# Optimization experiments

Measured on AMD Instinct MI355X. Metric: run time of the kernel, lower is better.

Reference implementation:

```python
import jax, jax.numpy as jnp
import numpy as np

H = 2            # attention heads
HID = 128        # hidden_channels
NEG_SLOPE = 0.2  # GATConv leaky_relu slope

N_USER, N_POST, N_ENT = 100000, 50000, 20000
TEXT_D, USER_D, ENT_D = 768, 64, 64
E_PUB, E_REP, E_CON, E_INT, E_FOL = 150000, 300000, 200000, 500000, 500000


def _gat(h_src, h_dst, src, dst, Wsrc, Wdst, asrc, adst, bias):
    """PyG GATConv((-1,-1), C, heads=H, concat=False, add_self_loops=False)."""
    n_dst = h_dst.shape[0]
    C = Wsrc.shape[1] // H
    xs = (h_src @ Wsrc).reshape(-1, H, C)          # [Ns,H,C]
    xd = (h_dst @ Wdst).reshape(-1, H, C)          # [Nd,H,C]
    al_s = jnp.einsum('nhc,hc->nh', xs, asrc)      # [Ns,H]
    al_d = jnp.einsum('nhc,hc->nh', xd, adst)      # [Nd,H]
    e = jax.nn.leaky_relu(al_s[src] + al_d[dst], NEG_SLOPE)   # [E,H]
    m = jax.ops.segment_max(e, dst, num_segments=n_dst)
    m = jnp.where(jnp.isfinite(m), m, 0.0)
    ex = jnp.exp(e - m[dst])
    denom = jax.ops.segment_sum(ex, dst, num_segments=n_dst)
    alpha = ex / (denom[dst] + 1e-16)              # per-dst softmax
    msg = xs[src] * alpha[:, :, None]              # [E,H,C]
    out = jax.ops.segment_sum(msg, dst, num_segments=n_dst)   # [Nd,H,C]
    return out.mean(axis=1) + bias                 # concat=False -> head mean


def setup_inputs() -> dict:
    key = jax.random.key(0)
    ks = jax.random.split(key, 24)
    s = 0.05
    d = {
        'post_cls': jax.random.normal(ks[0], (N_POST, TEXT_D), jnp.float32),
        'user_x': jax.random.normal(ks[1], (N_USER, USER_D), jnp.float32),
        'entity_x': jax.random.normal(ks[2], (N_ENT, ENT_D), jnp.float32),
        'Wpost': jax.random.normal(ks[3], (TEXT_D, HID), jnp.float32) * s,
        'bpost': jnp.zeros((HID,), jnp.float32),
        'Wuser': jax.random.normal(ks[4], (USER_D, HID), jnp.float32) * s,
        'buser': jnp.zeros((HID,), jnp.float32),
        'Went': jax.random.normal(ks[5], (ENT_D, HID), jnp.float32) * s,
        'bent': jnp.zeros((HID,), jnp.float32),
        # 2 layers x 5 relations (publish, repost, contain, interact, follow)
        'gat_Wsrc': jax.random.normal(ks[6], (2, 5, HID, H * HID), jnp.float32) * s,
        'gat_Wdst': jax.random.normal(ks[7], (2, 5, HID, H * HID), jnp.float32) * s,
        'gat_asrc': jax.random.normal(ks[8], (2, 5, H, HID), jnp.float32) * s,
        'gat_adst': jax.random.normal(ks[9], (2, 5, H, HID), jnp.float32) * s,
        'gat_bias': jnp.zeros((2, 5, HID), jnp.float32),
        'Wc1': jax.random.normal(ks[10], (HID, HID // 2), jnp.float32) * s,
        'bc1': jnp.zeros((HID // 2,), jnp.float32),
        'Wc2': jax.random.normal(ks[11], (HID // 2, 1), jnp.float32) * s,
        'bc2': jnp.zeros((1,), jnp.float32),
        'pub_src': jax.random.randint(ks[12], (E_PUB,), 0, N_USER, jnp.int32),
        'pub_dst': jax.random.randint(ks[13], (E_PUB,), 0, N_POST, jnp.int32),
        'rep_src': jax.random.randint(ks[14], (E_REP,), 0, N_USER, jnp.int32),
        'rep_dst': jax.random.randint(ks[15], (E_REP,), 0, N_POST, jnp.int32),
        'con_src': jax.random.randint(ks[16], (E_CON,), 0, N_POST, jnp.int32),
        'con_dst': jax.random.randint(ks[17], (E_CON,), 0, N_ENT, jnp.int32),
        'int_src': jax.random.randint(ks[18], (E_INT,), 0, N_USER, jnp.int32),
        'int_dst': jax.random.randint(ks[19], (E_INT,), 0, N_USER, jnp.int32),
        'fol_src': jax.random.randint(ks[20], (E_FOL,), 0, N_USER, jnp.int32),
        'fol_dst': jax.random.randint(ks[21], (E_FOL,), 0, N_USER, jnp.int32),
    }
    return d


def _forward(post_cls, user_x, entity_x, Wpost, bpost, Wuser, buser, Went, bent,
             gat_Wsrc, gat_Wdst, gat_asrc, gat_adst, gat_bias,
             Wc1, bc1, Wc2, bc2, edges):
    h = {
        'post': post_cls @ Wpost + bpost,
        'user': user_x @ Wuser + buser,
        'entity': entity_x @ Went + bent,
    }
    for l in range(2):
        def g(r, h_src, h_dst, src, dst):
            return _gat(h_src, h_dst, src, dst,
                        gat_Wsrc[l, r], gat_Wdst[l, r],
                        gat_asrc[l, r], gat_adst[l, r], gat_bias[l, r])
        # HeteroConv aggr='sum' over edge types sharing a dst node type
        new_post = (g(0, h['user'], h['post'], edges['pub_src'], edges['pub_dst'])
                    + g(1, h['user'], h['post'], edges['rep_src'], edges['rep_dst']))
        new_ent = g(2, h['post'], h['entity'], edges['con_src'], edges['con_dst'])
        new_user = (g(3, h['user'], h['user'], edges['int_src'], edges['int_dst'])
                    + g(4, h['user'], h['user'], edges['fol_src'], edges['fol_dst']))
        h = {'post': jax.nn.relu(new_post),
             'user': jax.nn.relu(new_user),
             'entity': jax.nn.relu(new_ent)}
    # classifier (dropout inactive at inference)
    z = jax.nn.relu(h['post'] @ Wc1 + bc1)
    out = z @ Wc2 + bc2
    return out.squeeze(-1)   # [n_posts]


def reference(post_cls, user_x, entity_x, Wpost, bpost, Wuser, buser, Went, bent,
              gat_Wsrc, gat_Wdst, gat_asrc, gat_adst, gat_bias,
              Wc1, bc1, Wc2, bc2,
              pub_src, pub_dst, rep_src, rep_dst, con_src, con_dst,
              int_src, int_dst, fol_src, fol_dst):
    edges = dict(pub_src=pub_src, pub_dst=pub_dst, rep_src=rep_src, rep_dst=rep_dst,
                 con_src=con_src, con_dst=con_dst, int_src=int_src, int_dst=int_dst,
                 fol_src=fol_src, fol_dst=fol_dst)
    return _forward(post_cls, user_x, entity_x, Wpost, bpost, Wuser, buser, Went, bent,
                    gat_Wsrc, gat_Wdst, gat_asrc, gat_adst, gat_bias,
                    Wc1, bc1, Wc2, bc2, edges)
```

## Files before the change

kernel.cpp:

```cpp
#include <hip/hip_runtime.h>
#include <cstdint>
#include <cstddef>

#define N_USER 100000
#define N_POST 50000
#define TEXT_D 768
#define USER_D 64
#define E_PUB 150000
#define E_REP 300000
#define E_INT 500000
#define E_FOL 500000
#define E_TOT 1450000
#define N_TOT 300000

typedef unsigned short ushort_t;
typedef float f4v __attribute__((ext_vector_type(4)));
typedef short s8v __attribute__((ext_vector_type(8)));
typedef unsigned short u4v __attribute__((ext_vector_type(4)));

__device__ __forceinline__ float leaky(float v) { return v > 0.f ? v : 0.2f * v; }
__device__ __forceinline__ void split_bf(float x, ushort_t& hi, ushort_t& lo) {
  unsigned u = __float_as_uint(x);
  hi = (ushort_t)(u >> 16);
  float r = x - __uint_as_float(u & 0xFFFF0000u);
  lo = (ushort_t)(__float_as_uint(r) >> 16);
}

struct Ptrs4 { const int* p[4]; };

__global__ void wvec_kernel(const float* __restrict__ W, const float* __restrict__ av,
                            float* __restrict__ wv) {
  int b = blockIdx.x;
  int lr = b / 2, h = b % 2;
  const float* Wp = W + ((size_t)lr * 128 * 256) + (size_t)threadIdx.x * 256 + h * 128;
  const float* ap = av + (size_t)(lr * 2 + h) * 128;
  float acc = 0.f;
  for (int c = 0; c < 128; ++c) acc += Wp[c] * ap[c];
  wv[(size_t)(lr * 2 + h) * 128 + threadIdx.x] = acc;
}

__global__ void wt_prep(const float* __restrict__ W, ushort_t* __restrict__ WTh,
                        ushort_t* __restrict__ WTl, int K, int C) {
  int k = blockIdx.x * 256 + threadIdx.x;
  int c = blockIdx.y;
  if (k >= K) return;
  ushort_t h, l;
  split_bf(W[(size_t)k * C + c], h, l);
  WTh[(size_t)c * K + k] = h;
  WTl[(size_t)c * K + k] = l;
}

__global__ void stk_prep(const float* __restrict__ Wa, const float* __restrict__ Wb,
                         ushort_t* __restrict__ STh, ushort_t* __restrict__ STl) {
  int rel = blockIdx.x;
  int c = blockIdx.y;
  int t = threadIdx.x;
  const float* W = rel ? Wb : Wa;
  float v = W[(size_t)(t & 127) * 256 + (size_t)(t >> 7) * 128 + c];
  ushort_t hh, ll;
  split_bf(v, hh, ll);
  size_t idx = (size_t)c * 512 + (size_t)rel * 256 + t;
  STh[idx] = hh;
  STl[idx] = ll;
}

__global__ void bias_sum(const float* __restrict__ gbias, float* __restrict__ BS) {
  int c = threadIdx.x;
  BS[c]       = gbias[0 * 640 + 0 * 128 + c] + gbias[0 * 640 + 1 * 128 + c];
  BS[128 + c] = gbias[0 * 640 + 3 * 128 + c] + gbias[0 * 640 + 4 * 128 + c];
  BS[256 + c] = gbias[1 * 640 + 0 * 128 + c] + gbias[1 * 640 + 1 * 128 + c];
}

template <int CF, bool BIAS, bool RELU>
__global__ __launch_bounds__(256) void gemm_mfma(const float* __restrict__ X,
                                                 const ushort_t* __restrict__ WTh,
                                                 const ushort_t* __restrict__ WTl,
                                                 const float* __restrict__ bv,
                                                 float* __restrict__ Out,
                                                 int N, int K) {
  __shared__ ushort_t Ah[64][32], Al[64][32];
  __shared__ ushort_t Bh[CF * 16][32], Bl[CF * 16][32];
  int t = threadIdx.x;
  int L = t & 63;
  int wv = t >> 6;
  int m = L & 15, quad = L >> 4;
  int row0 = blockIdx.x * 64;

  f4v acc[CF];
#pragma unroll
  for (int cf = 0; cf < CF; ++cf) acc[cf] = (f4v){0.f, 0.f, 0.f, 0.f};

  int nk = K >> 5;
  for (int kb = 0; kb < nk; ++kb) {
    int k0 = kb * 32;
#pragma unroll
    for (int i = 0; i < 2; ++i) {
      int s = t + 256 * i;
      int r = s >> 3, k4 = s & 7;
      int row = row0 + r;
      float4 v = make_float4(0.f, 0.f, 0.f, 0.f);
      if (row < N) v = *(const float4*)(X + (size_t)row * K + k0 + k4 * 4);
      ushort_t hx, lx, hy, ly, hz, lz, hw, lw;
      split_bf(v.x, hx, lx); split_bf(v.y, hy, ly);
      split_bf(v.z, hz, lz); split_bf(v.w, hw, lw);
      u4v h, l;
      h[0] = hx; h[1] = hy; h[2] = hz; h[3] = hw;
      l[0] = lx; l[1] = ly; l[2] = lz; l[3] = lw;
      *(u4v*)&Ah[r][k4 * 4] = h;
      *(u4v*)&Al[r][k4 * 4] = l;
    }
#pragma unroll
    for (int i = 0; i < CF / 4; ++i) {
      int s = t + 256 * i;
      int c = s >> 2, ch = s & 3;
      *(s8v*)&Bh[c][ch * 8] = *(const s8v*)(WTh + (size_t)c * K + k0 + ch * 8);
      *(s8v*)&Bl[c][ch * 8] = *(const s8v*)(WTl + (size_t)c * K + k0 + ch * 8);
    }
    __syncthreads();
    s8v a_h = *(const s8v*)&Ah[wv * 16 + m][quad * 8];
    s8v a_l = *(const s8v*)&Al[wv * 16 + m][quad * 8];
#pragma unroll
    for (int cf = 0; cf < CF; ++cf) {
      s8v b_h = *(const s8v*)&Bh[cf * 16 + m][quad * 8];
      s8v b_l = *(const s8v*)&Bl[cf * 16 + m][quad * 8];
      acc[cf] = __builtin_amdgcn_mfma_f32_16x16x32_bf16(a_h, b_h, acc[cf], 0, 0, 0);
      acc[cf] = __builtin_amdgcn_mfma_f32_16x16x32_bf16(a_h, b_l, acc[cf], 0, 0, 0);
      acc[cf] = __builtin_amdgcn_mfma_f32_16x16x32_bf16(a_l, b_h, acc[cf], 0, 0, 0);
    }
    __syncthreads();
  }

  float bvs[CF];
#pragma unroll
  for (int cf = 0; cf < CF; ++cf) bvs[cf] = BIAS ? bv[cf * 16 + m] : 0.f;
#pragma unroll
  for (int j = 0; j < 4; ++j) {
    int row = row0 + wv * 16 + quad * 4 + j;
    if (row < N) {
      float* o = Out + (size_t)row * (CF * 16) + m;
#pragma unroll
      for (int cf = 0; cf < CF; ++cf) {
        float vv = acc[cf][j] + bvs[cf];
        if (RELU) vv = fmaxf(vv, 0.f);
        o[cf * 16] = vv;
      }
    }
  }
}

__device__ __forceinline__ void rel_of(int g, int& r, int& loc, int& nb) {
  if (g < 450000) {
    if (g < 150000) { r = 0; loc = g;          nb = 0; }
    else            { r = 1; loc = g - 150000; nb = 50000; }
  } else if (g < 950000)  { r = 2; loc = g - 450000;  nb = 100000; }
  else                    { r = 3; loc = g - 950000;  nb = 200000; }
}
__global__ void histc_kernel(Ptrs4 dsts, int* __restrict__ cnt) {
  int g = blockIdx.x * 256 + threadIdx.x;
  if (g >= E_TOT) return;
  int r, loc, nb;
  rel_of(g, r, loc, nb);
  atomicAdd(&cnt[nb + dsts.p[r][loc]], 1);
}
__global__ __launch_bounds__(256) void scan1_kernel(const int* __restrict__ cnt,
                                                    int* __restrict__ excl,
                                                    int* __restrict__ partials, int Nd) {
  __shared__ int sb[256];
  int t = threadIdx.x;
  int base = blockIdx.x * 1024 + t * 4;
  int v[4];
#pragma unroll
  for (int j = 0; j < 4; ++j) v[j] = (base + j < Nd) ? cnt[base + j] : 0;
  int tot = v[0] + v[1] + v[2] + v[3];
  sb[t] = tot;
  __syncthreads();
  for (int off = 1; off < 256; off <<= 1) {
    int x = 0;
    if (t >= off) x = sb[t - off];
    __syncthreads();
    sb[t] += x;
    __syncthreads();
  }
  int ex = sb[t] - tot;
  if (t == 255) partials[blockIdx.x] = sb[t];
  int run = ex;
#pragma unroll
  for (int j = 0; j < 4; ++j) {
    if (base + j < Nd) excl[base + j] = run;
    run += v[j];
  }
}
__global__ __launch_bounds__(512) void scan2_kernel(int* __restrict__ partials, int B) {
  __shared__ int sb[512];
  int t = threadIdx.x;
  int v = (t < B) ? partials[t] : 0;
  sb[t] = v;
  __syncthreads();
  for (int off = 1; off < 512; off <<= 1) {
    int x = 0;
    if (t >= off) x = sb[t - off];
    __syncthreads();
    sb[t] += x;
    __syncthreads();
  }
  if (t < B) partials[t] = sb[t] - v;
}
__global__ void scan3_kernel(const int* __restrict__ excl, const int* __restrict__ partials,
                             int* __restrict__ rowptr, int* __restrict__ cursor) {
  int i = blockIdx.x * 256 + threadIdx.x;
  if (i < N_TOT) {
    int v = excl[i] + partials[i >> 10];
    rowptr[i] = v;
    cursor[i] = v;
  }
  if (i == 0) rowptr[N_TOT] = E_TOT;
}
__global__ void scatterc_kernel(Ptrs4 srcs, Ptrs4 dsts,
                                int* __restrict__ cursor, int* __restrict__ csrc) {
  int g = blockIdx.x * 256 + threadIdx.x;
  if (g >= E_TOT) return;
  int r, loc, nb;
  rel_of(g, r, loc, nb);
  int p = atomicAdd(&cursor[nb + dsts.p[r][loc]], 1);
  csrc[p] = srcs.p[r][loc];
}

__global__ __launch_bounds__(256) void logits2_kernel(const float* __restrict__ H,
                                                      const float* __restrict__ wsA,
                                                      const float* __restrict__ wsB,
                                                      float* __restrict__ alsA,
                                                      float* __restrict__ alsB, int Ns) {
  int n = blockIdx.x * 4 + (threadIdx.x >> 6);
  int lane = threadIdx.x & 63;
  if (n >= Ns) return;
  const float* hr = H + (size_t)n * 128;
  float ha = hr[lane], hb = hr[lane + 64];
  float p0 = ha * wsA[lane] + hb * wsA[lane + 64];
  float p1 = ha * wsA[128 + lane] + hb * wsA[192 + lane];
  float p2 = ha * wsB[lane] + hb * wsB[lane + 64];
  float p3 = ha * wsB[128 + lane] + hb * wsB[192 + lane];
#pragma unroll
  for (int mk = 32; mk; mk >>= 1) {
    p0 += __shfl_xor(p0, mk); p1 += __shfl_xor(p1, mk);
    p2 += __shfl_xor(p2, mk); p3 += __shfl_xor(p3, mk);
  }
  if (lane == 0) {
    *(float2*)(alsA + 2 * (size_t)n) = make_float2(p0, p1);
    *(float2*)(alsB + 2 * (size_t)n) = make_float2(p2, p3);
  }
}

__device__ __forceinline__ void dst_tvals(const float* __restrict__ Hd, const float* __restrict__ wdv,
                                          int d, int lane, float& t0, float& t1) {
  const float* hr = Hd + (size_t)d * 128;
  float ha = hr[lane], hb = hr[lane + 64];
  t0 = ha * wdv[lane] + hb * wdv[lane + 64];
  t1 = ha * wdv[128 + lane] + hb * wdv[192 + lane];
#pragma unroll
  for (int mk = 32; mk; mk >>= 1) { t0 += __shfl_xor(t0, mk); t1 += __shfl_xor(t1, mk); }
}

__device__ __forceinline__ void aggG_rel(const int* __restrict__ rowptr,
                                         const int* __restrict__ csrc,
                                         const float* __restrict__ als,
                                         const float* __restrict__ Hs,
                                         float t0, float t1, int d, int h, int s,
                                         int lane, float* __restrict__ Grow) {
  int start = rowptr[d], end = rowptr[d + 1];
  float den0 = 0.f, den1 = 0.f;
  float a0[4] = {0.f, 0.f, 0.f, 0.f}, a1[4] = {0.f, 0.f, 0.f, 0.f};
  if (end > start) {
    int last = end - 1;
    for (int b0 = start; b0 < end; b0 += 4) {
      int eA = b0 + h, eB = b0 + 2 + h;
      bool vA = eA < end, vB = eB < end;
      eA = vA ? eA : last;
      eB = vB ? eB : last;
      int sA = csrc[eA], sB = csrc[eB];
      float2 alA = *(const float2*)(als + 2 * (size_t)sA);
      float2 alB = *(const float2*)(als + 2 * (size_t)sB);
      f4v xA = *(const f4v*)(Hs + (size_t)sA * 128 + 4 * s);
      f4v xB = *(const f4v*)(Hs + (size_t)sB * 128 + 4 * s);
      float wA0 = vA ? __expf(leaky(alA.x + t0)) : 0.f;
      float wA1 = vA ? __expf(leaky(alA.y + t1)) : 0.f;
      float wB0 = vB ? __expf(leaky(alB.x + t0)) : 0.f;
      float wB1 = vB ? __expf(leaky(alB.y + t1)) : 0.f;
      den0 += wA0 + wB0;
      den1 += wA1 + wB1;
#pragma unroll
      for (int j = 0; j < 4; ++j) {
        a0[j] += wA0 * xA[j] + wB0 * xB[j];
        a1[j] += wA1 * xA[j] + wB1 * xB[j];
      }
    }
  }
  den0 += __shfl_xor(den0, 32);
  den1 += __shfl_xor(den1, 32);
  float i0 = 0.5f / (den0 + 1e-16f);
  float i1 = 0.5f / (den1 + 1e-16f);
  f4v o0, o1;
#pragma unroll
  for (int j = 0; j < 4; ++j) {
    float u = a0[j] + __shfl_xor(a0[j], 32);
    float v = a1[j] + __shfl_xor(a1[j], 32);
    o0[j] = u * i0;
    o1[j] = v * i1;
  }
  if (lane < 32) {
    *(f4v*)(Grow + 4 * s) = o0;
    *(f4v*)(Grow + 128 + 4 * s) = o1;
  }
}

__global__ __launch_bounds__(256) void aggG2_kernel(const int* __restrict__ rowA,
                                                    const int* __restrict__ rowB,
                                                    const int* __restrict__ csrc,
                                                    const float* __restrict__ alsA,
                                                    const float* __restrict__ alsB,
                                                    const float* __restrict__ wdvA,
                                                    const float* __restrict__ wdvB,
                                                    const float* __restrict__ Hs,
                                                    const float* __restrict__ Hd,
                                                    float* __restrict__ G,
                                                    int Nd, int dOff) {
  int dl = blockIdx.x * 4 + (threadIdx.x >> 6);
  int lane = threadIdx.x & 63;
  if (dl >= Nd) return;
  int d = dl + dOff;
  float tA0, tA1, tB0, tB1;
  dst_tvals(Hd, wdvA, d, lane, tA0, tA1);
  dst_tvals(Hd, wdvB, d, lane, tB0, tB1);
  int h = lane >> 5, s = lane & 31;
  float* Grow = G + (size_t)dl * 512;
  aggG_rel(rowA, csrc, alsA, Hs, tA0, tA1, d, h, s, lane, Grow);
  aggG_rel(rowB, csrc, alsB, Hs, tB0, tB1, d, h, s, lane, Grow + 256);
}

__global__ __launch_bounds__(256) void classifier_kernel(const float* __restrict__ Hp,
                                                         const float* __restrict__ Wc1, const float* __restrict__ bc1,
                                                         const float* __restrict__ Wc2, const float* __restrict__ bc2,
                                                         float* __restrict__ out, int N) {
  __shared__ float sW[128 * 64];
  int t = threadIdx.x;
#pragma unroll
  for (int i = 0; i < 8; ++i) ((float4*)sW)[t + 256 * i] = ((const float4*)Wc1)[t + 256 * i];
  __syncthreads();
  int lane = t & 63, wv = t >> 6;
  float b = bc1[lane], w2 = Wc2[lane], b2 = bc2[0];
#pragma unroll
  for (int nn = 0; nn < 2; ++nn) {
    int n = blockIdx.x * 8 + wv * 2 + nn;
    if (n >= N) continue;
    const float* hr = Hp + (size_t)n * 128;
    float accz = b;
    for (int k = 0; k < 128; ++k) accz += hr[k] * sW[k * 64 + lane];
    float z = fmaxf(accz, 0.f) * w2;
#pragma unroll
    for (int off = 32; off; off >>= 1) z += __shfl_down(z, off);
    if (lane == 0) out[n] = z + b2;
  }
}

extern "C" void kernel_launch(void* const* d_in, const int* in_sizes, int n_in,
                              void* d_out, int out_size, void* d_ws, size_t ws_size,
                              hipStream_t stream) {
  const float* post_cls = (const float*)d_in[0];
  const float* user_x   = (const float*)d_in[1];
  const float* Wpost = (const float*)d_in[3];
  const float* bpost = (const float*)d_in[4];
  const float* Wuser = (const float*)d_in[5];
  const float* buser = (const float*)d_in[6];
  const float* gWsrc = (const float*)d_in[9];
  const float* gWdst = (const float*)d_in[10];
  const float* gasrc = (const float*)d_in[11];
  const float* gadst = (const float*)d_in[12];
  const float* gbias = (const float*)d_in[13];
  const float* Wc1 = (const float*)d_in[14];
  const float* bc1 = (const float*)d_in[15];
  const float* Wc2 = (const float*)d_in[16];
  const float* bc2 = (const float*)d_in[17];
  Ptrs4 SRCS, DSTS;
  SRCS.p[0] = (const int*)d_in[18]; DSTS.p[0] = (const int*)d_in[19];
  SRCS.p[1] = (const int*)d_in[20]; DSTS.p[1] = (const int*)d_in[21];
  SRCS.p[2] = (const int*)d_in[24]; DSTS.p[2] = (const int*)d_in[25];
  SRCS.p[3] = (const int*)d_in[26]; DSTS.p[3] = (const int*)d_in[27];
  float* out = (float*)d_out;
  (void)ws_size; (void)in_sizes; (void)n_in; (void)out_size;

  float* Wf = (float*)d_ws;
  size_t o = 0;
  float* WDSTV = Wf + o; o += 2560;
  float* WSRCV = Wf + o; o += 2560;
  float* BS    = Wf + o; o += 384;
  float* ALSa  = Wf + o; o += (size_t)N_USER * 2;
  float* ALSb  = Wf + o; o += (size_t)N_USER * 2;
  float* HU    = Wf + o; o += (size_t)N_USER * 128;
  float* HP    = Wf + o; o += (size_t)N_POST * 128;
  float* G     = Wf + o; o += (size_t)N_POST * 512;
  float* TMP   = Wf + o; o += (size_t)N_POST * 128;
  int* Wi = (int*)(Wf + o);
  size_t io = 0;
  int* RP   = Wi + io; io += N_TOT + 1;
  int* CURS = Wi + io; io += N_TOT;
  int* CNT  = Wi + io; io += N_TOT;
  int* EXCL = Wi + io; io += N_TOT;
  int* PART = Wi + io; io += 512;
  int* CSRC = Wi + io; io += E_TOT;
  io = (io + 7) & ~(size_t)7;
  ushort_t* Wu = (ushort_t*)(Wi + io);
  size_t uo = 0;
  ushort_t* PWh = Wu + uo; uo += 128 * TEXT_D;
  ushort_t* PWl = Wu + uo; uo += 128 * TEXT_D;
  ushort_t* UWh = Wu + uo; uo += 128 * USER_D;
  ushort_t* UWl = Wu + uo; uo += 128 * USER_D;
  ushort_t* STh[3]; ushort_t* STl[3];
  for (int i = 0; i < 3; ++i) {
    STh[i] = Wu + uo; uo += 128 * 512;
    STl[i] = Wu + uo; uo += 128 * 512;
  }

  const int NOFF_PUB = 0, NOFF_REP = 50000, NOFF_INT = 100000, NOFF_FOL = 200000;

  (void)hipMemsetAsync(CNT, 0, (size_t)N_TOT * sizeof(int), stream);
  histc_kernel<<<(E_TOT + 255) / 256, 256, 0, stream>>>(DSTS, CNT);
  int B = (N_TOT + 1023) / 1024;
  scan1_kernel<<<B, 256, 0, stream>>>(CNT, EXCL, PART, N_TOT);
  scan2_kernel<<<1, 512, 0, stream>>>(PART, B);
  scan3_kernel<<<(N_TOT + 255) / 256, 256, 0, stream>>>(EXCL, PART, RP, CURS);
  scatterc_kernel<<<(E_TOT + 255) / 256, 256, 0, stream>>>(SRCS, DSTS, CURS, CSRC);

  wt_prep<<<dim3(3, 128), 256, 0, stream>>>(Wpost, PWh, PWl, TEXT_D, 128);
  wt_prep<<<dim3(1, 128), 256, 0, stream>>>(Wuser, UWh, UWl, USER_D, 128);
  stk_prep<<<dim3(2, 128), 256, 0, stream>>>(gWsrc + (size_t)0 * 32768, gWsrc + (size_t)1 * 32768, STh[0], STl[0]);
  stk_prep<<<dim3(2, 128), 256, 0, stream>>>(gWsrc + (size_t)3 * 32768, gWsrc + (size_t)4 * 32768, STh[1], STl[1]);
  stk_prep<<<dim3(2, 128), 256, 0, stream>>>(gWsrc + (size_t)5 * 32768, gWsrc + (size_t)6 * 32768, STh[2], STl[2]);
  wvec_kernel<<<20, 128, 0, stream>>>(gWdst, gadst, WDSTV);
  wvec_kernel<<<20, 128, 0, stream>>>(gWsrc, gasrc, WSRCV);
  bias_sum<<<1, 128, 0, stream>>>(gbias, BS);

  gemm_mfma<8, true, false><<<(N_POST + 63) / 64, 256, 0, stream>>>(
      post_cls, PWh, PWl, bpost, HP, N_POST, TEXT_D);
  gemm_mfma<8, true, false><<<(N_USER + 63) / 64, 256, 0, stream>>>(
      user_x, UWh, UWl, buser, HU, N_USER, USER_D);

  logits2_kernel<<<(N_USER + 3) / 4, 256, 0, stream>>>(
      HU, WSRCV + 0 * 256, WSRCV + 1 * 256, ALSa, ALSb, N_USER);
  aggG2_kernel<<<(N_POST + 3) / 4, 256, 0, stream>>>(
      RP + NOFF_PUB, RP + NOFF_REP, CSRC, ALSa, ALSb,
      WDSTV + 0 * 256, WDSTV + 1 * 256, HU, HP, G, N_POST, 0);
  gemm_mfma<8, true, true><<<(N_POST + 63) / 64, 256, 0, stream>>>(
      G, STh[0], STl[0], BS + 0, HP, N_POST, 512);

  logits2_kernel<<<(N_USER + 3) / 4, 256, 0, stream>>>(
      HU, WSRCV + 3 * 256, WSRCV + 4 * 256, ALSa, ALSb, N_USER);
  aggG2_kernel<<<(50000 + 3) / 4, 256, 0, stream>>>(
      RP + NOFF_INT, RP + NOFF_FOL, CSRC, ALSa, ALSb,
      WDSTV + 3 * 256, WDSTV + 4 * 256, HU, HU, G, 50000, 0);
  gemm_mfma<8, true, true><<<(50000 + 63) / 64, 256, 0, stream>>>(
      G, STh[1], STl[1], BS + 128, TMP, 50000, 512);
  aggG2_kernel<<<(50000 + 3) / 4, 256, 0, stream>>>(
      RP + NOFF_INT, RP + NOFF_FOL, CSRC, ALSa, ALSb,
      WDSTV + 3 * 256, WDSTV + 4 * 256, HU, HU, G, 50000, 50000);
  gemm_mfma<8, true, true><<<(50000 + 63) / 64, 256, 0, stream>>>(
      G, STh[1], STl[1], BS + 128, HU + (size_t)50000 * 128, 50000, 512);
  (void)hipMemcpyAsync(HU, TMP, (size_t)50000 * 128 * sizeof(float),
                       hipMemcpyDeviceToDevice, stream);

  logits2_kernel<<<(N_USER + 3) / 4, 256, 0, stream>>>(
      HU, WSRCV + 5 * 256, WSRCV + 6 * 256, ALSa, ALSb, N_USER);
  aggG2_kernel<<<(N_POST + 3) / 4, 256, 0, stream>>>(
      RP + NOFF_PUB, RP + NOFF_REP, CSRC, ALSa, ALSb,
      WDSTV + 5 * 256, WDSTV + 6 * 256, HU, HP, G, N_POST, 0);
  gemm_mfma<8, true, true><<<(N_POST + 63) / 64, 256, 0, stream>>>(
      G, STh[2], STl[2], BS + 256, HP, N_POST, 512);

  classifier_kernel<<<(N_POST + 7) / 8, 256, 0, stream>>>(HP, Wc1, bc1, Wc2, bc2, out, N_POST);
}
```

Baseline: 1.096 ms.

## Pre-split aggregated features to bf16 hi/lo and add swizzled prefetching GEMM

The aggregation kernel now writes its output directly as bf16 hi/lo halves, so the following K=512 GEMM no longer has to split fp32 into two bf16 parts on every tile load. A new gemm_split kernel uses 64-wide K tiles, XOR-swizzled LDS, a 2x2 wave layout with register prefetch of the next tile, and a fused bias+ReLU epilogue. The aggregation kernel gives each wave a single relation and unrolls eight edges per iteration for more memory-level parallelism. The old GEMM pads its LDS rows to 40 to reduce bank conflicts. The cost is larger code and more register pressure in the new GEMM.

```diff
diff --git a/kernel.cpp b/kernel.cpp
--- a/kernel.cpp
+++ b/kernel.cpp
@@ -6,10 +6,6 @@
 #define N_POST 50000
 #define TEXT_D 768
 #define USER_D 64
-#define E_PUB 150000
-#define E_REP 300000
-#define E_INT 500000
-#define E_FOL 500000
 #define E_TOT 1450000
 #define N_TOT 300000
 
@@ -17,6 +13,7 @@
 typedef float f4v __attribute__((ext_vector_type(4)));
 typedef short s8v __attribute__((ext_vector_type(8)));
 typedef unsigned short u4v __attribute__((ext_vector_type(4)));
+typedef unsigned short u8v __attribute__((ext_vector_type(8)));
 
 __device__ __forceinline__ float leaky(float v) { return v > 0.f ? v : 0.2f * v; }
 __device__ __forceinline__ void split_bf(float x, ushort_t& hi, ushort_t& lo) {
@@ -71,15 +68,15 @@
   BS[256 + c] = gbias[1 * 640 + 0 * 128 + c] + gbias[1 * 640 + 1 * 128 + c];
 }
 
-template <int CF, bool BIAS, bool RELU>
+template <int CF, bool BIAS>
 __global__ __launch_bounds__(256) void gemm_mfma(const float* __restrict__ X,
                                                  const ushort_t* __restrict__ WTh,
                                                  const ushort_t* __restrict__ WTl,
                                                  const float* __restrict__ bv,
                                                  float* __restrict__ Out,
                                                  int N, int K) {
-  __shared__ ushort_t Ah[64][32], Al[64][32];
-  __shared__ ushort_t Bh[CF * 16][32], Bl[CF * 16][32];
+  __shared__ ushort_t Ah[64][40], Al[64][40];
+  __shared__ ushort_t Bh[CF * 16][40], Bl[CF * 16][40];
   int t = threadIdx.x;
   int L = t & 63;
   int wv = t >> 6;
@@ -113,8 +110,8 @@
     for (int i = 0; i < CF / 4; ++i) {
       int s = t + 256 * i;
       int c = s >> 2, ch = s & 3;
-      *(s8v*)&Bh[c][ch * 8] = *(const s8v*)(WTh + (size_t)c * K + k0 + ch * 8);
-      *(s8v*)&Bl[c][ch * 8] = *(const s8v*)(WTl + (size_t)c * K + k0 + ch * 8);
+      *(u8v*)&Bh[c][ch * 8] = *(const u8v*)(WTh + (size_t)c * K + k0 + ch * 8);
+      *(u8v*)&Bl[c][ch * 8] = *(const u8v*)(WTl + (size_t)c * K + k0 + ch * 8);
     }
     __syncthreads();
     s8v a_h = *(const s8v*)&Ah[wv * 16 + m][quad * 8];
@@ -139,13 +136,120 @@
     if (row < N) {
       float* o = Out + (size_t)row * (CF * 16) + m;
 #pragma unroll
-      for (int cf = 0; cf < CF; ++cf) {
-        float vv = acc[cf][j] + bvs[cf];
-        if (RELU) vv = fmaxf(vv, 0.f);
-        o[cf * 16] = vv;
+      for (int cf = 0; cf < CF; ++cf) o[cf * 16] = acc[cf][j] + bvs[cf];
+    }
+  }
+}
+
+template <int NK>
+__global__ __launch_bounds__(256) void gemm_split(const ushort_t* __restrict__ Agh,
+                                                  const ushort_t* __restrict__ Agl,
+                                                  const ushort_t* __restrict__ Bgh,
+                                                  const ushort_t* __restrict__ Bgl,
+                                                  const float* __restrict__ bv,
+                                                  float* __restrict__ Out, int N) {
+  constexpr int K = NK * 64;
+  __shared__ __align__(16) ushort_t LAh[64 * 64], LAl[64 * 64];
+  __shared__ __align__(16) ushort_t LBh[128 * 64], LBl[128 * 64];
+  int t = threadIdx.x;
+  int lane = t & 63, w = t >> 6;
+  int m = lane & 15, quad = lane >> 4;
+  int wr = w >> 1, wc = w & 1;
+  int row0 = blockIdx.x * 64;
+
+  int arow[2], acol[2];
+#pragma unroll
+  for (int i = 0; i < 2; ++i) {
+    int p = t + 256 * i;
+    int r = p >> 3, q = (p & 7) ^ (r & 7);
+    int row = row0 + r;
+    if (row >= N) row = N - 1;
+    arow[i] = row; acol[i] = q * 8;
+  }
+  int bcol[4], bq[4];
+#pragma unroll
+  for (int i = 0; i < 4; ++i) {
+    int p = t + 256 * i;
+    int c = p >> 3, q = (p & 7) ^ (c & 7);
+    bcol[i] = c; bq[i] = q * 8;
+  }
+
+  f4v acc[2][4];
+#pragma unroll
+  for (int mt = 0; mt < 2; ++mt)
+#pragma unroll
+    for (int ct = 0; ct < 4; ++ct) acc[mt][ct] = (f4v){0.f, 0.f, 0.f, 0.f};
+
+  u8v rah[2], ral[2], rbh[4], rbl[4];
+  auto LOAD = [&](int kb) {
+    int k0 = kb * 64;
+#pragma unroll
+    for (int i = 0; i < 2; ++i) {
+      rah[i] = *(const u8v*)(Agh + (size_t)arow[i] * K + k0 + acol[i]);
+      ral[i] = *(const u8v*)(Agl + (size_t)arow[i] * K + k0 + acol[i]);
+    }
+#pragma unroll
+    for (int i = 0; i < 4; ++i) {
+      rbh[i] = *(const u8v*)(Bgh + (size_t)bcol[i] * K + k0 + bq[i]);
+      rbl[i] = *(const u8v*)(Bgl + (size_t)bcol[i] * K + k0 + bq[i]);
+    }
+  };
+  LOAD(0);
+  for (int kb = 0; kb < NK; ++kb) {
+    __syncthreads();
+#pragma unroll
+    for (int i = 0; i < 2; ++i) {
+      *(u8v*)&LAh[(size_t)(t + 256 * i) * 8] = rah[i];
+      *(u8v*)&LAl[(size_t)(t + 256 * i) * 8] = ral[i];
+    }
+#pragma unroll
+    for (int i = 0; i < 4; ++i) {
+      *(u8v*)&LBh[(size_t)(t + 256 * i) * 8] = rbh[i];
+      *(u8v*)&LBl[(size_t)(t + 256 * i) * 8] = rbl[i];
+    }
+    __syncthreads();
+    if (kb + 1 < NK) LOAD(kb + 1);
+#pragma unroll
+    for (int ks = 0; ks < 2; ++ks) {
+      s8v ah[2], alo[2], bh[4], blo[4];
+#pragma unroll
+      for (int mt = 0; mt < 2; ++mt) {
+        int r = wr * 32 + mt * 16 + m;
+        int gr = r * 8 + ((ks * 4 + quad) ^ (m & 7));
+        ah[mt] = *(const s8v*)&LAh[(size_t)gr * 8];
+        alo[mt] = *(const s8v*)&LAl[(size_t)gr * 8];
       }
-    }
-  }
+#pragma unroll
+      for (int ct = 0; ct < 4; ++ct) {
+        int c = wc * 64 + ct * 16 + m;
+        int gc = c * 8 + ((ks * 4 + quad) ^ (m & 7));
+        bh[ct] = *(const s8v*)&LBh[(size_t)gc * 8];
+        blo[ct] = *(const s8v*)&LBl[(size_t)gc * 8];
+      }
+#pragma unroll
+      for (int mt = 0; mt < 2; ++mt)
+#pragma unroll
+        for (int ct = 0; ct < 4; ++ct) {
+          acc[mt][ct] = __builtin_amdgcn_mfma_f32_16x16x32_bf16(ah[mt], bh[ct], acc[mt][ct], 0, 0, 0);
+          acc[mt][ct] = __builtin_amdgcn_mfma_f32_16x16x32_bf16(ah[mt], blo[ct], acc[mt][ct], 0, 0, 0);
+          acc[mt][ct] = __builtin_amdgcn_mfma_f32_16x16x32_bf16(alo[mt], bh[ct], acc[mt][ct], 0, 0, 0);
+        }
+    }
+  }
+  float bb[4];
+#pragma unroll
+  for (int ct = 0; ct < 4; ++ct) bb[ct] = bv[wc * 64 + ct * 16 + m];
+#pragma unroll
+  for (int mt = 0; mt < 2; ++mt)
+#pragma unroll
+    for (int j = 0; j < 4; ++j) {
+      int row = row0 + wr * 32 + mt * 16 + quad * 4 + j;
+      if (row < N) {
+        float* o = Out + (size_t)row * 128 + wc * 64 + m;
+#pragma unroll
+        for (int ct = 0; ct < 4; ++ct) o[ct * 16] = fmaxf(acc[mt][ct][j] + bb[ct], 0.f);
+      }
+    }
 }
 
 __device__ __forceinline__ void rel_of(int g, int& r, int& loc, int& nb) {
@@ -265,32 +369,39 @@
                                          const float* __restrict__ als,
                                          const float* __restrict__ Hs,
                                          float t0, float t1, int d, int h, int s,
-                                         int lane, float* __restrict__ Grow) {
+                                         int lane, ushort_t* __restrict__ GrowH,
+                                         ushort_t* __restrict__ GrowL) {
   int start = rowptr[d], end = rowptr[d + 1];
   float den0 = 0.f, den1 = 0.f;
   float a0[4] = {0.f, 0.f, 0.f, 0.f}, a1[4] = {0.f, 0.f, 0.f, 0.f};
   if (end > start) {
     int last = end - 1;
-    for (int b0 = start; b0 < end; b0 += 4) {
-      int eA = b0 + h, eB = b0 + 2 + h;
-      bool vA = eA < end, vB = eB < end;
-      eA = vA ? eA : last;
-      eB = vB ? eB : last;
-      int sA = csrc[eA], sB = csrc[eB];
-      float2 alA = *(const float2*)(als + 2 * (size_t)sA);
-      float2 alB = *(const float2*)(als + 2 * (size_t)sB);
-      f4v xA = *(const f4v*)(Hs + (size_t)sA * 128 + 4 * s);
-      f4v xB = *(const f4v*)(Hs + (size_t)sB * 128 + 4 * s);
-      float wA0 = vA ? __expf(leaky(alA.x + t0)) : 0.f;
-      float wA1 = vA ? __expf(leaky(alA.y + t1)) : 0.f;
-      float wB0 = vB ? __expf(leaky(alB.x + t0)) : 0.f;
-      float wB1 = vB ? __expf(leaky(alB.y + t1)) : 0.f;
-      den0 += wA0 + wB0;
-      den1 += wA1 + wB1;
+    for (int b0 = start; b0 < end; b0 += 8) {
+      int e[4]; bool vl[4]; int sid[4];
 #pragma unroll
       for (int j = 0; j < 4; ++j) {
-        a0[j] += wA0 * xA[j] + wB0 * xB[j];
-        a1[j] += wA1 * xA[j] + wB1 * xB[j];
+        int ee = b0 + 2 * j + h;
+        vl[j] = ee < end;
+        e[j] = vl[j] ? ee : last;
+      }
+#pragma unroll
+      for (int j = 0; j < 4; ++j) sid[j] = csrc[e[j]];
+      float2 al[4]; f4v x[4];
+#pragma unroll
+      for (int j = 0; j < 4; ++j) {
+        al[j] = *(const float2*)(als + 2 * (size_t)sid[j]);
+        x[j] = *(const f4v*)(Hs + (size_t)sid[j] * 128 + 4 * s);
+      }
+#pragma unroll
+      for (int j = 0; j < 4; ++j) {
+        float w0 = vl[j] ? __expf(leaky(al[j].x + t0)) : 0.f;
+        float w1 = vl[j] ? __expf(leaky(al[j].y + t1)) : 0.f;
+        den0 += w0; den1 += w1;
+#pragma unroll
+        for (int q = 0; q < 4; ++q) {
+          a0[q] += w0 * x[j][q];
+          a1[q] += w1 * x[j][q];
+        }
       }
     }
   }
@@ -300,15 +411,24 @@
   float i1 = 0.5f / (den1 + 1e-16f);
   f4v o0, o1;
 #pragma unroll
-  for (int j = 0; j < 4; ++j) {
-    float u = a0[j] + __shfl_xor(a0[j], 32);
-    float v = a1[j] + __shfl_xor(a1[j], 32);
-    o0[j] = u * i0;
-    o1[j] = v * i1;
+  for (int q = 0; q < 4; ++q) {
+    float u = a0[q] + __shfl_xor(a0[q], 32);
+    float v = a1[q] + __shfl_xor(a1[q], 32);
+    o0[q] = u * i0;
+    o1[q] = v * i1;
   }
   if (lane < 32) {
-    *(f4v*)(Grow + 4 * s) = o0;
-    *(f4v*)(Grow + 128 + 4 * s) = o1;
+    u4v g0h, g0l, g1h, g1l;
+#pragma unroll
+    for (int q = 0; q < 4; ++q) {
+      ushort_t hh, ll;
+      split_bf(o0[q], hh, ll); g0h[q] = hh; g0l[q] = ll;
+      split_bf(o1[q], hh, ll); g1h[q] = hh; g1l[q] = ll;
+    }
+    *(u4v*)(GrowH + 4 * s) = g0h;
+    *(u4v*)(GrowL + 4 * s) = g0l;
+    *(u4v*)(GrowH + 128 + 4 * s) = g1h;
+    *(u4v*)(GrowL + 128 + 4 * s) = g1l;
   }
 }
 
@@ -321,19 +441,23 @@
                                                     const float* __restrict__ wdvB,
                                                     const float* __restrict__ Hs,
                                                     const float* __restrict__ Hd,
-                                                    float* __restrict__ G,
+                                                    ushort_t* __restrict__ Gh,
+                                                    ushort_t* __restrict__ Gl,
                                                     int Nd, int dOff) {
-  int dl = blockIdx.x * 4 + (threadIdx.x >> 6);
+  int w = threadIdx.x >> 6;
   int lane = threadIdx.x & 63;
+  int dl = blockIdx.x * 2 + (w >> 1);
+  int rel = w & 1;
   if (dl >= Nd) return;
   int d = dl + dOff;
-  float tA0, tA1, tB0, tB1;
-  dst_tvals(Hd, wdvA, d, lane, tA0, tA1);
-  dst_tvals(Hd, wdvB, d, lane, tB0, tB1);
+  const int* rp = rel ? rowB : rowA;
+  const float* alsP = rel ? alsB : alsA;
+  const float* wdv = rel ? wdvB : wdvA;
+  float t0, t1;
+  dst_tvals(Hd, wdv, d, lane, t0, t1);
   int h = lane >> 5, s = lane & 31;
-  float* Grow = G + (size_t)dl * 512;
-  aggG_rel(rowA, csrc, alsA, Hs, tA0, tA1, d, h, s, lane, Grow);
-  aggG_rel(rowB, csrc, alsB, Hs, tB0, tB1, d, h, s, lane, Grow + 256);
+  aggG_rel(rp, csrc, alsP, Hs, t0, t1, d, h, s, lane,
+           Gh + (size_t)dl * 512 + rel * 256, Gl + (size_t)dl * 512 + rel * 256);
 }
 
 __global__ __launch_bounds__(256) void classifier_kernel(const float* __restrict__ Hp,
@@ -396,7 +520,6 @@
   float* ALSb  = Wf + o; o += (size_t)N_USER * 2;
   float* HU    = Wf + o; o += (size_t)N_USER * 128;
   float* HP    = Wf + o; o += (size_t)N_POST * 128;
-  float* G     = Wf + o; o += (size_t)N_POST * 512;
   float* TMP   = Wf + o; o += (size_t)N_POST * 128;
   int* Wi = (int*)(Wf + o);
   size_t io = 0;
@@ -418,6 +541,8 @@
     STh[i] = Wu + uo; uo += 128 * 512;
     STl[i] = Wu + uo; uo += 128 * 512;
   }
+  ushort_t* Gh = Wu + uo; uo += (size_t)N_POST * 512;
+  ushort_t* Gl = Wu + uo; uo += (size_t)N_POST * 512;
 
   const int NOFF_PUB = 0, NOFF_REP = 50000, NOFF_INT = 100000, NOFF_FOL = 200000;
 
@@ -438,41 +563,41 @@
   wvec_kernel<<<20, 128, 0, stream>>>(gWsrc, gasrc, WSRCV);
   bias_sum<<<1, 128, 0, stream>>>(gbias, BS);
 
-  gemm_mfma<8, true, false><<<(N_POST + 63) / 64, 256, 0, stream>>>(
+  gemm_mfma<8, true><<<(N_POST + 63) / 64, 256, 0, stream>>>(
       post_cls, PWh, PWl, bpost, HP, N_POST, TEXT_D);
-  gemm_mfma<8, true, false><<<(N_USER + 63) / 64, 256, 0, stream>>>(
+  gemm_mfma<8, true><<<(N_USER + 63) / 64, 256, 0, stream>>>(
       user_x, UWh, UWl, buser, HU, N_USER, USER_D);
 
   logits2_kernel<<<(N_USER + 3) / 4, 256, 0, stream>>>(
       HU, WSRCV + 0 * 256, WSRCV + 1 * 256, ALSa, ALSb, N_USER);
-  aggG2_kernel<<<(N_POST + 3) / 4, 256, 0, stream>>>(
+  aggG2_kernel<<<(N_POST + 1) / 2, 256, 0, stream>>>(
       RP + NOFF_PUB, RP + NOFF_REP, CSRC, ALSa, ALSb,
-      WDSTV + 0 * 256, WDSTV + 1 * 256, HU, HP, G, N_POST, 0);
-  gemm_mfma<8, true, true><<<(N_POST + 63) / 64, 256, 0, stream>>>(
-      G, STh[0], STl[0], BS + 0, HP, N_POST, 512);
+      WDSTV + 0 * 256, WDSTV + 1 * 256, HU, HP, Gh, Gl, N_POST, 0);
+  gemm_split<8><<<(N_POST + 63) / 64, 256, 0, stream>>>(
+      Gh, Gl, STh[0], STl[0], BS + 0, HP, N_POST);
 
   logits2_kernel<<<(N_USER + 3) / 4, 256, 0, stream>>>(
       HU, WSRCV + 3 * 256, WSRCV + 4 * 256, ALSa, ALSb, N_USER);
-  aggG2_kernel<<<(50000 + 3) / 4, 256, 0, stream>>>(
+  aggG2_kernel<<<(50000 + 1) / 2, 256, 0, stream>>>(
       RP + NOFF_INT, RP + NOFF_FOL, CSRC, ALSa, ALSb,
-      WDSTV + 3 * 256, WDSTV + 4 * 256, HU, HU, G, 50000, 0);
-  gemm_mfma<8, true, true><<<(50000 + 63) / 64, 256, 0, stream>>>(
-      G, STh[1], STl[1], BS + 128, TMP, 50000, 512);
-  aggG2_kernel<<<(50000 + 3) / 4, 256, 0, stream>>>(
+      WDSTV + 3 * 256, WDSTV + 4 * 256, HU, HU, Gh, Gl, 50000, 0);
+  gemm_split<8><<<(50000 + 63) / 64, 256, 0, stream>>>(
+      Gh, Gl, STh[1], STl[1], BS + 128, TMP, 50000);
+  aggG2_kernel<<<(50000 + 1) / 2, 256, 0, stream>>>(
       RP + NOFF_INT, RP + NOFF_FOL, CSRC, ALSa, ALSb,
-      WDSTV + 3 * 256, WDSTV + 4 * 256, HU, HU, G, 50000, 50000);
-  gemm_mfma<8, true, true><<<(50000 + 63) / 64, 256, 0, stream>>>(
-      G, STh[1], STl[1], BS + 128, HU + (size_t)50000 * 128, 50000, 512);
+      WDSTV + 3 * 256, WDSTV + 4 * 256, HU, HU, Gh, Gl, 50000, 50000);
+  gemm_split<8><<<(50000 + 63) / 64, 256, 0, stream>>>(
+      Gh, Gl, STh[1], STl[1], BS + 128, HU + (size_t)50000 * 128, 50000);
   (void)hipMemcpyAsync(HU, TMP, (size_t)50000 * 128 * sizeof(float),
                        hipMemcpyDeviceToDevice, stream);
 
   logits2_kernel<<<(N_USER + 3) / 4, 256, 0, stream>>>(
       HU, WSRCV + 5 * 256, WSRCV + 6 * 256, ALSa, ALSb, N_USER);
-  aggG2_kernel<<<(N_POST + 3) / 4, 256, 0, stream>>>(
+  aggG2_kernel<<<(N_POST + 1) / 2, 256, 0, stream>>>(
       RP + NOFF_PUB, RP + NOFF_REP, CSRC, ALSa, ALSb,
-      WDSTV + 5 * 256, WDSTV + 6 * 256, HU, HP, G, N_POST, 0);
-  gemm_mfma<8, true, true><<<(N_POST + 63) / 64, 256, 0, stream>>>(
-      G, STh[2], STl[2], BS + 256, HP, N_POST, 512);
+      WDSTV + 5 * 256, WDSTV + 6 * 256, HU, HP, Gh, Gl, N_POST, 0);
+  gemm_split<8><<<(N_POST + 63) / 64, 256, 0, stream>>>(
+      Gh, Gl, STh[2], STl[2], BS + 256, HP, N_POST);
 
   classifier_kernel<<<(N_POST + 7) / 8, 256, 0, stream>>>(HP, Wc1, bc1, Wc2, bc2, out, N_POST);
 }
```

Result: faster. 1.067 ms (median of 2 runs) (-2.7%).
